# Kernel optimization log

Hardware: AMD Instinct MI355X
Metric: run time of the kernel (lower is better)

## Reference

```python
import jax, jax.numpy as jnp
import numpy as np

B, OBS, PRED, E, H = 32768, 9, 8, 128, 128


def setup_inputs() -> dict:
    key = jax.random.key(0)
    ks = jax.random.split(key, 20)
    s = 0.1
    def n(k, shape):
        return jax.random.normal(k, shape, jnp.float32) * s
    return dict(
        obs=jax.random.normal(ks[0], (B, OBS, 4), jnp.float32),
        hidden=jnp.zeros((1, B, H), jnp.float32),
        W_le=n(ks[1], (E, 2)), b_le=n(ks[2], (E,)),
        W_ve=n(ks[3], (E, 2)), b_ve=n(ks[4], (E,)),
        Wih_l=n(ks[5], (3 * H, E)), Whh_l=n(ks[6], (3 * H, H)),
        bih_l=n(ks[7], (3 * H,)), bhh_l=n(ks[8], (3 * H,)),
        Wih_v=n(ks[9], (3 * H, E)), Whh_v=n(ks[10], (3 * H, H)),
        bih_v=n(ks[11], (3 * H,)), bhh_v=n(ks[12], (3 * H,)),
        W_lo=n(ks[13], (2, H)), b_lo=n(ks[14], (2,)),
        W_vo=n(ks[15], (2, H)), b_vo=n(ks[16], (2,)),
        W_at=n(ks[17], (2, 4)), b_at=n(ks[18], (2,)),
    )


def reference(obs, hidden, W_le, b_le, W_ve, b_ve,
              Wih_l, Whh_l, bih_l, bhh_l,
              Wih_v, Whh_v, bih_v, bhh_v,
              W_lo, b_lo, W_vo, b_vo, W_at, b_at):
    h0 = hidden[0]  # [B, H]

    def gru(x, h, Wih, Whh, bih, bhh):
        # PyTorch GRUCell math, gate order r,z,n
        gi = x @ Wih.T + bih
        gh = h @ Whh.T + bhh
        ir, iz, inn = jnp.split(gi, 3, axis=-1)
        hr, hz, hn = jnp.split(gh, 3, axis=-1)
        r = jax.nn.sigmoid(ir + hr)
        z = jax.nn.sigmoid(iz + hz)
        nn_ = jnp.tanh(inn + r * hn)
        return (1.0 - z) * nn_ + z * h

    def run_seq(seq, h, W_e, b_e, Wih, Whh, bih, bhh):
        # seq: [B, T, 2] -> relu embed then scan GRU over time
        emb = jax.nn.relu(jnp.einsum('btc,ec->bte', seq, W_e) + b_e)
        def step(hc, xt):
            return gru(xt, hc, Wih, Whh, bih, bhh), None
        h, _ = jax.lax.scan(step, h, jnp.swapaxes(emb, 0, 1))
        return h  # last output == last hidden for 1-layer GRU

    def one_time(x_seq, h_loc, h_vel):
        loc, vel = x_seq[..., :2], x_seq[..., 2:]
        h_loc = run_seq(loc, h_loc, W_le, b_le, Wih_l, Whh_l, bih_l, bhh_l)
        h_vel = run_seq(vel, h_vel, W_ve, b_ve, Wih_v, Whh_v, bih_v, bhh_v)
        pred = jnp.concatenate([h_loc @ W_lo.T + b_lo,
                                h_vel @ W_vo.T + b_vo], axis=-1)  # [B,4]
        attw = jax.nn.softmax(pred @ W_at.T + b_at, axis=-1)       # [B,2]
        last_in = jnp.concatenate([loc[:, -1], vel[:, -1]], axis=-1)  # [B,4]
        return last_in, pred, h_loc, h_vel, attw

    def tweak(li, lp, aw):
        al, av = aw[:, 0:1], aw[:, 1:2]
        x0, y0 = li[:, 0:1], li[:, 1:2]
        x1, y1, u1, v1 = lp[:, 0:1], lp[:, 1:2], lp[:, 2:3], lp[:, 3:4]
        nx = al * x1 + av * (x0 + u1)
        ny = al * y1 + av * (y0 + v1)
        nu, nv = nx - x0, ny - y0
        return (jnp.concatenate([nx, ny, nu, nv], axis=-1),
                jnp.concatenate([nx, ny], axis=-1))

    li, lp, hl, hv, aw = one_time(obs, h0, h0)
    a, out = tweak(li, lp, aw)
    preds = []
    for _ in range(PRED):
        li, lp, hl, hv, aw = one_time(a[:, None, :], hl, hv)
        a, out = tweak(li, lp, aw)
        preds.append(out)
    return jnp.stack(preds, axis=1)  # [B, PRED, 2]
```

## Files before the change

### kernel.cpp

```cpp
#include <hip/hip_runtime.h>
#include <hip/hip_bf16.h>


typedef __attribute__((ext_vector_type(8))) short short8;
typedef __attribute__((ext_vector_type(4))) float float4v;

#define NB 32768

#define OFF_EMBF 0
#define OFF_HF   65536
#define OFF_WE   131072
#define OFF_BIAS 135168
#define OFF_WOP  139264
#define OFF_PART 141312
#define OFF_PRED 149504
#define OFF_A    151552
#define OFF_AT   153600
#define DYN_LDS  153664

__device__ __forceinline__ ushort bfc(float x) {
  uint u = __builtin_bit_cast(uint, x);
  uint r = (u + 0x7fffu + ((u >> 16) & 1u)) >> 16;
  return (ushort)r;
}
__device__ __forceinline__ float bf2f(ushort b) {
  return __builtin_bit_cast(float, (uint)b << 16);
}
__device__ __forceinline__ float4v mfma16(short8 a, short8 b, float4v c) {
  return __builtin_amdgcn_mfma_f32_16x16x32_bf16(a, b, c, 0, 0, 0);
}
__device__ __forceinline__ float sigm(float x) {
  return __fdividef(1.0f, 1.0f + __expf(-x));
}
__device__ __forceinline__ float tanh_(float x) {
  return 1.0f - __fdividef(2.0f, 1.0f + __expf(2.0f * x));
}

__device__ __host__ __forceinline__ int kmap(int g, int p) {
  return (p < 4) ? (4 * g + p) : (16 + 4 * g + (p - 4));
}

__global__ void pack_w(const float* __restrict__ w0, const float* __restrict__ w1,
                       const float* __restrict__ w2, const float* __restrict__ w3,
                       short8* __restrict__ outp) {
  int t = blockIdx.x * 256 + threadIdx.x;
  if (t >= 4 * 96 * 64) return;
  int lane = t & 63;
  int tile = (t >> 6) % 96;
  int mat = t / 6144;
  const float* W = (mat == 0) ? w0 : (mat == 1) ? w1 : (mat == 2) ? w2 : w3;
  int mt = tile >> 2, kt = tile & 3;
  int g = lane >> 4, q = lane & 15;
  int row = mt * 16 + q;
  union { ushort u[8]; short8 v; } pw;
#pragma unroll
  for (int p = 0; p < 8; ++p) {
    int k = kt * 32 + kmap(g, p);
    pw.u[p] = bfc(W[row * 128 + k]);
  }
  outp[t] = pw.v;
}

__global__ __launch_bounds__(512, 2) void lvatt_main(
    const float* __restrict__ obs, const float* __restrict__ hidden,
    const float* __restrict__ W_le, const float* __restrict__ b_le,
    const float* __restrict__ W_ve, const float* __restrict__ b_ve,
    const float* __restrict__ bih_l, const float* __restrict__ bhh_l,
    const float* __restrict__ bih_v, const float* __restrict__ bhh_v,
    const float* __restrict__ W_lo, const float* __restrict__ b_lo,
    const float* __restrict__ W_vo, const float* __restrict__ b_vo,
    const float* __restrict__ W_at, const float* __restrict__ b_at,
    const short8* __restrict__ wpack, float* __restrict__ out) {
  extern __shared__ char smem[];
  short8* embF = (short8*)(smem + OFF_EMBF);
  short8* hF = (short8*)(smem + OFF_HF);
  float* s_we = (float*)(smem + OFF_WE);
  float* s_bias = (float*)(smem + OFF_BIAS);
  float* s_wop = (float*)(smem + OFF_WOP);
  float* s_part = (float*)(smem + OFF_PART);
  float* s_pred = (float*)(smem + OFF_PRED);
  float* s_a = (float*)(smem + OFF_A);
  float* s_at = (float*)(smem + OFF_AT);

  const int tid = threadIdx.x;
  const int lane = tid & 63;
  const int g = (lane >> 4) & 3;
  const int q = lane & 15;
  const int wv = tid >> 6;
  const int gru = wv & 1;
  const int j = wv >> 1;
  const int base = blockIdx.x * 128;

  if (tid < 128) {
    int col = tid;
    s_we[(0 * 128 + col) * 4 + 0] = W_le[col * 2];
    s_we[(0 * 128 + col) * 4 + 1] = W_le[col * 2 + 1];
    s_we[(0 * 128 + col) * 4 + 2] = b_le[col];
    s_we[(0 * 128 + col) * 4 + 3] = 0.f;
    s_we[(1 * 128 + col) * 4 + 0] = W_ve[col * 2];
    s_we[(1 * 128 + col) * 4 + 1] = W_ve[col * 2 + 1];
    s_we[(1 * 128 + col) * 4 + 2] = b_ve[col];
    s_we[(1 * 128 + col) * 4 + 3] = 0.f;
    s_bias[(0 * 4 + 0) * 128 + col] = bih_l[col] + bhh_l[col];
    s_bias[(0 * 4 + 1) * 128 + col] = bih_l[128 + col] + bhh_l[128 + col];
    s_bias[(0 * 4 + 2) * 128 + col] = bih_l[256 + col];
    s_bias[(0 * 4 + 3) * 128 + col] = bhh_l[256 + col];
    s_bias[(1 * 4 + 0) * 128 + col] = bih_v[col] + bhh_v[col];
    s_bias[(1 * 4 + 1) * 128 + col] = bih_v[128 + col] + bhh_v[128 + col];
    s_bias[(1 * 4 + 2) * 128 + col] = bih_v[256 + col];
    s_bias[(1 * 4 + 3) * 128 + col] = bhh_v[256 + col];
    s_wop[(0 * 128 + col) * 2 + 0] = W_lo[col];
    s_wop[(0 * 128 + col) * 2 + 1] = W_lo[128 + col];
    s_wop[(1 * 128 + col) * 2 + 0] = W_vo[col];
    s_wop[(1 * 128 + col) * 2 + 1] = W_vo[128 + col];
  }
  if (tid < 4) s_at[tid] = (tid < 2) ? b_lo[tid] : b_vo[tid - 2];
  else if (tid < 12) s_at[tid] = W_at[tid - 4];
  else if (tid < 14) s_at[tid] = b_at[tid - 12];

  short8 aih[3][2][4], ahh[3][2][4];
#pragma unroll
  for (int G = 0; G < 3; ++G)
#pragma unroll
    for (int c2 = 0; c2 < 2; ++c2)
#pragma unroll
      for (int kt = 0; kt < 4; ++kt) {
        int mt = G * 8 + 2 * j + c2;
        aih[G][c2][kt] = wpack[(size_t)(((gru * 2 + 0) * 96 + mt * 4 + kt) * 64 + lane)];
        ahh[G][c2][kt] = wpack[(size_t)(((gru * 2 + 1) * 96 + mt * 4 + kt) * 64 + lane)];
      }

#pragma unroll 1
  for (int nt = 0; nt < 8; ++nt) {
    const float* hp = hidden + (size_t)(base + nt * 16 + q) * 128 + 32 * j + 4 * g;
    float4v h0a = *(const float4v*)(hp);
    float4v h0b = *(const float4v*)(hp + 16);
    union { ushort u[8]; short8 v; } h8;
#pragma unroll
    for (int r = 0; r < 4; ++r) { h8.u[r] = bfc(h0a[r]); h8.u[4 + r] = bfc(h0b[r]); }
    hF[((gru * 8 + nt) * 4 + j) * 64 + lane] = h8.v;
  }
  __syncthreads();

#pragma unroll 1
  for (int t = 0; t < 17; ++t) {
    float4v wcol[8];
#pragma unroll
    for (int c2 = 0; c2 < 2; ++c2)
#pragma unroll
      for (int r = 0; r < 4; ++r) {
        int col = 32 * j + 16 * c2 + 4 * g + r;
        wcol[c2 * 4 + r] = *(const float4v*)&s_we[(gru * 128 + col) * 4];
      }
#pragma unroll 1
    for (int nt = 0; nt < 8; ++nt) {
      float x0, x1;
      if (t < 9) {
        const float* op = obs + (size_t)(base + nt * 16 + q) * 36 + t * 4 + 2 * gru;
        x0 = op[0]; x1 = op[1];
      } else {
        const float* ap = s_a + (nt * 16 + q) * 4 + 2 * gru;
        x0 = ap[0]; x1 = ap[1];
      }
      union { ushort u[8]; short8 v; } e8;
#pragma unroll
      for (int p = 0; p < 8; ++p)
        e8.u[p] = bfc(fmaxf(fmaf(wcol[p][0], x0, fmaf(wcol[p][1], x1, wcol[p][2])), 0.f));
      embF[((gru * 8 + nt) * 4 + j) * 64 + lane] = e8.v;
    }
    __syncthreads();

#pragma unroll 1
    for (int nt = 0; nt < 8; ++nt) {
      const int fb = (gru * 8 + nt) * 4;
      float4v racc[2], zacc[2], inacc[2], hnacc[2];
#pragma unroll
      for (int c2 = 0; c2 < 2; ++c2) {
        int colA = 32 * j + 16 * c2 + 4 * g;
        racc[c2] = *(const float4v*)&s_bias[(gru * 4 + 0) * 128 + colA];
        zacc[c2] = *(const float4v*)&s_bias[(gru * 4 + 1) * 128 + colA];
        inacc[c2] = *(const float4v*)&s_bias[(gru * 4 + 2) * 128 + colA];
        hnacc[c2] = *(const float4v*)&s_bias[(gru * 4 + 3) * 128 + colA];
      }
      short8 hj = hF[(fb + j) * 64 + lane];
#pragma unroll
      for (int kt = 0; kt < 4; ++kt) {
        short8 bE = embF[(fb + kt) * 64 + lane];
        short8 bH = hF[(fb + kt) * 64 + lane];
#pragma unroll
        for (int c2 = 0; c2 < 2; ++c2) {
          racc[c2] = mfma16(aih[0][c2][kt], bE, racc[c2]);
          racc[c2] = mfma16(ahh[0][c2][kt], bH, racc[c2]);
          zacc[c2] = mfma16(aih[1][c2][kt], bE, zacc[c2]);
          zacc[c2] = mfma16(ahh[1][c2][kt], bH, zacc[c2]);
          inacc[c2] = mfma16(aih[2][c2][kt], bE, inacc[c2]);
          hnacc[c2] = mfma16(ahh[2][c2][kt], bH, hnacc[c2]);
        }
      }
      union { ushort u[8]; short8 v; } hjv; hjv.v = hj;
      union { ushort u[8]; short8 v; } nh;
      float hnew[8];
#pragma unroll
      for (int c2 = 0; c2 < 2; ++c2)
#pragma unroll
        for (int r = 0; r < 4; ++r) {
          int p = c2 * 4 + r;
          float hold = bf2f(hjv.u[p]);
          float rr = sigm(racc[c2][r]);
          float zz = sigm(zacc[c2][r]);
          float nn = tanh_(fmaf(rr, hnacc[c2][r], inacc[c2][r]));
          float hv = fmaf(zz, hold - nn, nn);
          hnew[p] = hv;
          nh.u[p] = bfc(hv);
        }
      if (t >= 8) {
        float p0 = 0.f, p1 = 0.f;
#pragma unroll
        for (int c2 = 0; c2 < 2; ++c2) {
          int colA = 32 * j + 16 * c2 + 4 * g;
          float4v w01 = *(const float4v*)&s_wop[(gru * 128 + colA) * 2];
          float4v w23 = *(const float4v*)&s_wop[(gru * 128 + colA + 2) * 2];
          p0 += hnew[c2 * 4 + 0] * w01[0] + hnew[c2 * 4 + 1] * w01[2] +
                hnew[c2 * 4 + 2] * w23[0] + hnew[c2 * 4 + 3] * w23[2];
          p1 += hnew[c2 * 4 + 0] * w01[1] + hnew[c2 * 4 + 1] * w01[3] +
                hnew[c2 * 4 + 2] * w23[1] + hnew[c2 * 4 + 3] * w23[3];
        }
        p0 += __shfl_xor(p0, 16); p0 += __shfl_xor(p0, 32);
        p1 += __shfl_xor(p1, 16); p1 += __shfl_xor(p1, 32);
        if (lane < 16) {
          float2 pw; pw.x = p0; pw.y = p1;
          *(float2*)&s_part[(((gru * 4 + j) * 8 + nt) * 16 + q) * 2] = pw;
        }
      }
      __syncthreads();
      hF[(fb + j) * 64 + lane] = nh.v;
    }

    if (t >= 8) {
      {
        int b = tid >> 2, v = tid & 3;
        int gr = v >> 1, vv = v & 1;
        float s = s_at[v];
#pragma unroll
        for (int jj = 0; jj < 4; ++jj)
          s += s_part[(((gr * 4 + jj) * 8 + (b >> 4)) * 16 + (b & 15)) * 2 + vv];
        s_pred[b * 4 + v] = s;
      }
      __syncthreads();
      if (tid < 128) {
        int b = tid;
        float4v p = *(const float4v*)&s_pred[b * 4];
        float x0, y0;
        if (t == 8) {
          const float* op = obs + (size_t)(base + b) * 36 + 32;
          x0 = op[0]; y0 = op[1];
        } else {
          x0 = s_a[b * 4]; y0 = s_a[b * 4 + 1];
        }
        float t0 = fmaf(p[0], s_at[4], fmaf(p[1], s_at[5], fmaf(p[2], s_at[6], fmaf(p[3], s_at[7], s_at[12]))));
        float t1 = fmaf(p[0], s_at[8], fmaf(p[1], s_at[9], fmaf(p[2], s_at[10], fmaf(p[3], s_at[11], s_at[13]))));
        float al = sigm(t0 - t1);
        float av = 1.0f - al;
        float nx = al * p[0] + av * (x0 + p[2]);
        float ny = al * p[1] + av * (y0 + p[3]);
        float4v an; an[0] = nx; an[1] = ny; an[2] = nx - x0; an[3] = ny - y0;
        *(float4v*)&s_a[b * 4] = an;
        if (t > 8) {
          float2 o2; o2.x = nx; o2.y = ny;
          *(float2*)(out + (size_t)(base + b) * 16 + (t - 9) * 2) = o2;
        }
      }
      __syncthreads();
    }
  }
}

extern "C" void kernel_launch(void* const* d_in, const int* in_sizes, int n_in,
                              void* d_out, int out_size, void* d_ws, size_t ws_size,
                              hipStream_t stream) {
  const float* obs = (const float*)d_in[0];
  const float* hid = (const float*)d_in[1];
  const float* W_le = (const float*)d_in[2];
  const float* b_le = (const float*)d_in[3];
  const float* W_ve = (const float*)d_in[4];
  const float* b_ve = (const float*)d_in[5];
  const float* Wih_l = (const float*)d_in[6];
  const float* Whh_l = (const float*)d_in[7];
  const float* bih_l = (const float*)d_in[8];
  const float* bhh_l = (const float*)d_in[9];
  const float* Wih_v = (const float*)d_in[10];
  const float* Whh_v = (const float*)d_in[11];
  const float* bih_v = (const float*)d_in[12];
  const float* bhh_v = (const float*)d_in[13];
  const float* W_lo = (const float*)d_in[14];
  const float* b_lo = (const float*)d_in[15];
  const float* W_vo = (const float*)d_in[16];
  const float* b_vo = (const float*)d_in[17];
  const float* W_at = (const float*)d_in[18];
  const float* b_at = (const float*)d_in[19];

  short8* wp = (short8*)d_ws;

  hipFuncSetAttribute(reinterpret_cast<const void*>(lvatt_main),
                      hipFuncAttributeMaxDynamicSharedMemorySize, DYN_LDS);

  hipLaunchKernelGGL(pack_w, dim3(96), dim3(256), 0, stream,
                     Wih_l, Whh_l, Wih_v, Whh_v, wp);
  hipLaunchKernelGGL(lvatt_main, dim3(NB / 128), dim3(512), DYN_LDS, stream,
                     obs, hid, W_le, b_le, W_ve, b_ve,
                     bih_l, bhh_l, bih_v, bhh_v,
                     W_lo, b_lo, W_vo, b_vo, W_at, b_at,
                     (const short8*)wp, (float*)d_out);
}
```

Measured before the change: 423.3 us.

## Double-buffer hidden and embedding LDS tiles to drop per-tile barriers

Each block now processes its 128 rows as two sequential groups of 64. The hidden state and embedding fragments are ping-ponged between two LDS buffers indexed by timestep parity, which removes the __syncthreads inside every per-tile GRU iteration. The two-stage prediction reduction is merged into one pass run by 64 threads, dropping one barrier and the s_pred buffer. In exchange, the row groups run one after another within a block, so the fixed cost of 17 sequential steps is paid twice per block.

```diff
diff --git a/kernel.cpp b/kernel.cpp
--- a/kernel.cpp
+++ b/kernel.cpp
@@ -1,22 +1,22 @@
 #include <hip/hip_runtime.h>
-#include <hip/hip_bf16.h>
 
 
 typedef __attribute__((ext_vector_type(8))) short short8;
 typedef __attribute__((ext_vector_type(4))) float float4v;
+typedef __attribute__((ext_vector_type(2))) float float2v;
 
 #define NB 32768
+#define NT 4
 
 #define OFF_EMBF 0
 #define OFF_HF   65536
-#define OFF_WE   131072
-#define OFF_BIAS 135168
+#define OFF_BIAS 131072
+#define OFF_WE   135168
 #define OFF_WOP  139264
 #define OFF_PART 141312
-#define OFF_PRED 149504
-#define OFF_A    151552
-#define OFF_AT   153600
-#define DYN_LDS  153664
+#define OFF_A    145408
+#define OFF_AT   146432
+#define DYN_LDS  146496
 
 __device__ __forceinline__ ushort bfc(float x) {
   uint u = __builtin_bit_cast(uint, x);
@@ -61,7 +61,13 @@
   outp[t] = pw.v;
 }
 
-__global__ __launch_bounds__(512, 2) void lvatt_main(
+__device__ __forceinline__ int fidx(int buf, int gru, int nt, int kt) {
+  return (((buf * 2 + gru) * NT + nt) * 4 + kt) * 64;
+}
+
+__global__ __attribute__((amdgpu_flat_work_group_size(512, 512),
+                          amdgpu_waves_per_eu(2, 2)))
+void lvatt_main(
     const float* __restrict__ obs, const float* __restrict__ hidden,
     const float* __restrict__ W_le, const float* __restrict__ b_le,
     const float* __restrict__ W_ve, const float* __restrict__ b_ve,
@@ -74,11 +80,10 @@
   extern __shared__ char smem[];
   short8* embF = (short8*)(smem + OFF_EMBF);
   short8* hF = (short8*)(smem + OFF_HF);
+  float* s_bias = (float*)(smem + OFF_BIAS);
   float* s_we = (float*)(smem + OFF_WE);
-  float* s_bias = (float*)(smem + OFF_BIAS);
   float* s_wop = (float*)(smem + OFF_WOP);
   float* s_part = (float*)(smem + OFF_PART);
-  float* s_pred = (float*)(smem + OFF_PRED);
   float* s_a = (float*)(smem + OFF_A);
   float* s_at = (float*)(smem + OFF_AT);
 
@@ -89,7 +94,6 @@
   const int wv = tid >> 6;
   const int gru = wv & 1;
   const int j = wv >> 1;
-  const int base = blockIdx.x * 128;
 
   if (tid < 128) {
     int col = tid;
@@ -131,146 +135,150 @@
       }
 
 #pragma unroll 1
-  for (int nt = 0; nt < 8; ++nt) {
-    const float* hp = hidden + (size_t)(base + nt * 16 + q) * 128 + 32 * j + 4 * g;
-    float4v h0a = *(const float4v*)(hp);
-    float4v h0b = *(const float4v*)(hp + 16);
-    union { ushort u[8]; short8 v; } h8;
-#pragma unroll
-    for (int r = 0; r < 4; ++r) { h8.u[r] = bfc(h0a[r]); h8.u[4 + r] = bfc(h0b[r]); }
-    hF[((gru * 8 + nt) * 4 + j) * 64 + lane] = h8.v;
-  }
-  __syncthreads();
-
-#pragma unroll 1
-  for (int t = 0; t < 17; ++t) {
-    float4v wcol[8];
-#pragma unroll
-    for (int c2 = 0; c2 < 2; ++c2)
-#pragma unroll
-      for (int r = 0; r < 4; ++r) {
-        int col = 32 * j + 16 * c2 + 4 * g + r;
-        wcol[c2 * 4 + r] = *(const float4v*)&s_we[(gru * 128 + col) * 4];
-      }
-#pragma unroll 1
-    for (int nt = 0; nt < 8; ++nt) {
-      float x0, x1;
-      if (t < 9) {
-        const float* op = obs + (size_t)(base + nt * 16 + q) * 36 + t * 4 + 2 * gru;
-        x0 = op[0]; x1 = op[1];
-      } else {
-        const float* ap = s_a + (nt * 16 + q) * 4 + 2 * gru;
-        x0 = ap[0]; x1 = ap[1];
-      }
-      union { ushort u[8]; short8 v; } e8;
-#pragma unroll
-      for (int p = 0; p < 8; ++p)
-        e8.u[p] = bfc(fmaxf(fmaf(wcol[p][0], x0, fmaf(wcol[p][1], x1, wcol[p][2])), 0.f));
-      embF[((gru * 8 + nt) * 4 + j) * 64 + lane] = e8.v;
+  for (int rg = 0; rg < 2; ++rg) {
+    const int base = (blockIdx.x * 2 + rg) * 64;
+
+#pragma unroll
+    for (int nt = 0; nt < NT; ++nt) {
+      const float* hp = hidden + (size_t)(base + nt * 16 + q) * 128 + 32 * j + 4 * g;
+      float4v h0a = *(const float4v*)(hp);
+      float4v h0b = *(const float4v*)(hp + 16);
+      union { ushort u[8]; short8 v; } h8;
+#pragma unroll
+      for (int r = 0; r < 4; ++r) { h8.u[r] = bfc(h0a[r]); h8.u[4 + r] = bfc(h0b[r]); }
+      hF[fidx(0, gru, nt, j) + lane] = h8.v;
     }
     __syncthreads();
 
 #pragma unroll 1
-    for (int nt = 0; nt < 8; ++nt) {
-      const int fb = (gru * 8 + nt) * 4;
-      float4v racc[2], zacc[2], inacc[2], hnacc[2];
-#pragma unroll
-      for (int c2 = 0; c2 < 2; ++c2) {
-        int colA = 32 * j + 16 * c2 + 4 * g;
-        racc[c2] = *(const float4v*)&s_bias[(gru * 4 + 0) * 128 + colA];
-        zacc[c2] = *(const float4v*)&s_bias[(gru * 4 + 1) * 128 + colA];
-        inacc[c2] = *(const float4v*)&s_bias[(gru * 4 + 2) * 128 + colA];
-        hnacc[c2] = *(const float4v*)&s_bias[(gru * 4 + 3) * 128 + colA];
-      }
-      short8 hj = hF[(fb + j) * 64 + lane];
-#pragma unroll
-      for (int kt = 0; kt < 4; ++kt) {
-        short8 bE = embF[(fb + kt) * 64 + lane];
-        short8 bH = hF[(fb + kt) * 64 + lane];
-#pragma unroll
-        for (int c2 = 0; c2 < 2; ++c2) {
-          racc[c2] = mfma16(aih[0][c2][kt], bE, racc[c2]);
-          racc[c2] = mfma16(ahh[0][c2][kt], bH, racc[c2]);
-          zacc[c2] = mfma16(aih[1][c2][kt], bE, zacc[c2]);
-          zacc[c2] = mfma16(ahh[1][c2][kt], bH, zacc[c2]);
-          inacc[c2] = mfma16(aih[2][c2][kt], bE, inacc[c2]);
-          hnacc[c2] = mfma16(ahh[2][c2][kt], bH, hnacc[c2]);
-        }
-      }
-      union { ushort u[8]; short8 v; } hjv; hjv.v = hj;
-      union { ushort u[8]; short8 v; } nh;
-      float hnew[8];
-#pragma unroll
-      for (int c2 = 0; c2 < 2; ++c2)
-#pragma unroll
-        for (int r = 0; r < 4; ++r) {
-          int p = c2 * 4 + r;
-          float hold = bf2f(hjv.u[p]);
-          float rr = sigm(racc[c2][r]);
-          float zz = sigm(zacc[c2][r]);
-          float nn = tanh_(fmaf(rr, hnacc[c2][r], inacc[c2][r]));
-          float hv = fmaf(zz, hold - nn, nn);
-          hnew[p] = hv;
-          nh.u[p] = bfc(hv);
-        }
-      if (t >= 8) {
-        float p0 = 0.f, p1 = 0.f;
+    for (int t = 0; t < 17; ++t) {
+      const int tb = t & 1;
+
+      float4v wcol[8];
+#pragma unroll
+      for (int p = 0; p < 8; ++p) {
+        int col = 32 * j + 16 * (p >> 2) + 4 * g + (p & 3);
+        wcol[p] = *(const float4v*)&s_we[(gru * 128 + col) * 4];
+      }
+#pragma unroll
+      for (int nt = 0; nt < NT; ++nt) {
+        float x0, x1;
+        if (t < 9) {
+          const float2v o2 = *(const float2v*)(obs + (size_t)(base + nt * 16 + q) * 36 + t * 4 + 2 * gru);
+          x0 = o2[0]; x1 = o2[1];
+        } else {
+          const float2v a2 = *(const float2v*)(s_a + (nt * 16 + q) * 4 + 2 * gru);
+          x0 = a2[0]; x1 = a2[1];
+        }
+        union { ushort u[8]; short8 v; } e8;
+#pragma unroll
+        for (int p = 0; p < 8; ++p)
+          e8.u[p] = bfc(fmaxf(fmaf(wcol[p][0], x0, fmaf(wcol[p][1], x1, wcol[p][2])), 0.f));
+        embF[fidx(tb, gru, nt, j) + lane] = e8.v;
+      }
+      __syncthreads();
+
+#pragma unroll
+      for (int nt = 0; nt < NT; ++nt) {
+        float4v accr[2], accz[2], accin[2], acchn[2];
 #pragma unroll
         for (int c2 = 0; c2 < 2; ++c2) {
           int colA = 32 * j + 16 * c2 + 4 * g;
-          float4v w01 = *(const float4v*)&s_wop[(gru * 128 + colA) * 2];
-          float4v w23 = *(const float4v*)&s_wop[(gru * 128 + colA + 2) * 2];
-          p0 += hnew[c2 * 4 + 0] * w01[0] + hnew[c2 * 4 + 1] * w01[2] +
-                hnew[c2 * 4 + 2] * w23[0] + hnew[c2 * 4 + 3] * w23[2];
-          p1 += hnew[c2 * 4 + 0] * w01[1] + hnew[c2 * 4 + 1] * w01[3] +
-                hnew[c2 * 4 + 2] * w23[1] + hnew[c2 * 4 + 3] * w23[3];
-        }
-        p0 += __shfl_xor(p0, 16); p0 += __shfl_xor(p0, 32);
-        p1 += __shfl_xor(p1, 16); p1 += __shfl_xor(p1, 32);
-        if (lane < 16) {
-          float2 pw; pw.x = p0; pw.y = p1;
-          *(float2*)&s_part[(((gru * 4 + j) * 8 + nt) * 16 + q) * 2] = pw;
-        }
-      }
-      __syncthreads();
-      hF[(fb + j) * 64 + lane] = nh.v;
-    }
-
-    if (t >= 8) {
-      {
-        int b = tid >> 2, v = tid & 3;
-        int gr = v >> 1, vv = v & 1;
-        float s = s_at[v];
-#pragma unroll
-        for (int jj = 0; jj < 4; ++jj)
-          s += s_part[(((gr * 4 + jj) * 8 + (b >> 4)) * 16 + (b & 15)) * 2 + vv];
-        s_pred[b * 4 + v] = s;
-      }
-      __syncthreads();
-      if (tid < 128) {
-        int b = tid;
-        float4v p = *(const float4v*)&s_pred[b * 4];
-        float x0, y0;
-        if (t == 8) {
-          const float* op = obs + (size_t)(base + b) * 36 + 32;
-          x0 = op[0]; y0 = op[1];
-        } else {
-          x0 = s_a[b * 4]; y0 = s_a[b * 4 + 1];
-        }
-        float t0 = fmaf(p[0], s_at[4], fmaf(p[1], s_at[5], fmaf(p[2], s_at[6], fmaf(p[3], s_at[7], s_at[12]))));
-        float t1 = fmaf(p[0], s_at[8], fmaf(p[1], s_at[9], fmaf(p[2], s_at[10], fmaf(p[3], s_at[11], s_at[13]))));
-        float al = sigm(t0 - t1);
-        float av = 1.0f - al;
-        float nx = al * p[0] + av * (x0 + p[2]);
-        float ny = al * p[1] + av * (y0 + p[3]);
-        float4v an; an[0] = nx; an[1] = ny; an[2] = nx - x0; an[3] = ny - y0;
-        *(float4v*)&s_a[b * 4] = an;
-        if (t > 8) {
-          float2 o2; o2.x = nx; o2.y = ny;
-          *(float2*)(out + (size_t)(base + b) * 16 + (t - 9) * 2) = o2;
-        }
-      }
-      __syncthreads();
+          accr[c2] = *(const float4v*)&s_bias[(gru * 4 + 0) * 128 + colA];
+          accz[c2] = *(const float4v*)&s_bias[(gru * 4 + 1) * 128 + colA];
+          accin[c2] = *(const float4v*)&s_bias[(gru * 4 + 2) * 128 + colA];
+          acchn[c2] = *(const float4v*)&s_bias[(gru * 4 + 3) * 128 + colA];
+        }
+        short8 hj = hF[fidx(tb, gru, nt, j) + lane];
+#pragma unroll
+        for (int kt = 0; kt < 4; ++kt) {
+          short8 bE = embF[fidx(tb, gru, nt, kt) + lane];
+          short8 bH = hF[fidx(tb, gru, nt, kt) + lane];
+#pragma unroll
+          for (int c2 = 0; c2 < 2; ++c2) {
+            accr[c2] = mfma16(aih[0][c2][kt], bE, accr[c2]);
+            accr[c2] = mfma16(ahh[0][c2][kt], bH, accr[c2]);
+            accz[c2] = mfma16(aih[1][c2][kt], bE, accz[c2]);
+            accz[c2] = mfma16(ahh[1][c2][kt], bH, accz[c2]);
+            accin[c2] = mfma16(aih[2][c2][kt], bE, accin[c2]);
+            acchn[c2] = mfma16(ahh[2][c2][kt], bH, acchn[c2]);
+          }
+        }
+        union { ushort u[8]; short8 v; } hjv; hjv.v = hj;
+        union { ushort u[8]; short8 v; } nh;
+        float hnew[8];
+#pragma unroll
+        for (int c2 = 0; c2 < 2; ++c2)
+#pragma unroll
+          for (int r = 0; r < 4; ++r) {
+            int p = c2 * 4 + r;
+            float hold = bf2f(hjv.u[p]);
+            float rr = sigm(accr[c2][r]);
+            float zz = sigm(accz[c2][r]);
+            float nn = tanh_(fmaf(rr, acchn[c2][r], accin[c2][r]));
+            float hv = fmaf(zz, hold - nn, nn);
+            hnew[p] = hv;
+            nh.u[p] = bfc(hv);
+          }
+        hF[fidx(tb ^ 1, gru, nt, j) + lane] = nh.v;
+        if (t >= 8) {
+          float P0 = 0.f, P1 = 0.f;
+#pragma unroll
+          for (int c2 = 0; c2 < 2; ++c2) {
+            int colA = 32 * j + 16 * c2 + 4 * g;
+            float4v w01 = *(const float4v*)&s_wop[(gru * 128 + colA) * 2];
+            float4v w23 = *(const float4v*)&s_wop[(gru * 128 + colA + 2) * 2];
+            P0 += hnew[c2 * 4 + 0] * w01[0] + hnew[c2 * 4 + 1] * w01[2] +
+                  hnew[c2 * 4 + 2] * w23[0] + hnew[c2 * 4 + 3] * w23[2];
+            P1 += hnew[c2 * 4 + 0] * w01[1] + hnew[c2 * 4 + 1] * w01[3] +
+                  hnew[c2 * 4 + 2] * w23[1] + hnew[c2 * 4 + 3] * w23[3];
+          }
+          P0 += __shfl_xor(P0, 16); P0 += __shfl_xor(P0, 32);
+          P1 += __shfl_xor(P1, 16); P1 += __shfl_xor(P1, 32);
+          if (lane < 16) {
+            float2 pw; pw.x = P0; pw.y = P1;
+            *(float2*)&s_part[(((gru * 4 + j) * NT + nt) * 16 + q) * 2] = pw;
+          }
+        }
+      }
+
+      if (t >= 8) {
+        __syncthreads();
+        if (tid < 64) {
+          int b = tid;
+          int ntb = b >> 4, qb = b & 15;
+          float p[4];
+#pragma unroll
+          for (int v = 0; v < 4; ++v) {
+            int gr = v >> 1, vv = v & 1;
+            float s = s_at[v];
+#pragma unroll
+            for (int jj = 0; jj < 4; ++jj)
+              s += s_part[(((gr * 4 + jj) * NT + ntb) * 16 + qb) * 2 + vv];
+            p[v] = s;
+          }
+          float x0, y0;
+          if (t == 8) {
+            const float2v o2 = *(const float2v*)(obs + (size_t)(base + b) * 36 + 32);
+            x0 = o2[0]; y0 = o2[1];
+          } else {
+            x0 = s_a[b * 4]; y0 = s_a[b * 4 + 1];
+          }
+          float t0 = fmaf(p[0], s_at[4], fmaf(p[1], s_at[5], fmaf(p[2], s_at[6], fmaf(p[3], s_at[7], s_at[12]))));
+          float t1 = fmaf(p[0], s_at[8], fmaf(p[1], s_at[9], fmaf(p[2], s_at[10], fmaf(p[3], s_at[11], s_at[13]))));
+          float al = sigm(t0 - t1);
+          float av = 1.0f - al;
+          float nx = al * p[0] + av * (x0 + p[2]);
+          float ny = al * p[1] + av * (y0 + p[3]);
+          float4v an; an[0] = nx; an[1] = ny; an[2] = nx - x0; an[3] = ny - y0;
+          *(float4v*)&s_a[b * 4] = an;
+          if (t > 8) {
+            float2 o2; o2.x = nx; o2.y = ny;
+            *(float2*)(out + (size_t)(base + b) * 16 + (t - 9) * 2) = o2;
+          }
+        }
+        __syncthreads();
+      }
     }
   }
 }
```

Result: faster. 406.0 us (-4.1%).
